# Performance work log

Measured on AMD Instinct MI355X. Metric: run time of the kernel, lower is better.

## Reference

```python
import jax, jax.numpy as jnp
import numpy as np

B, HW, E = 64, 14, 512   # batch, feature-map side, encoder_dim
A = D = M = 512          # attention_dim, decoder_dim, embed_dim
V = 1000                 # vocab_size
L = 257                  # max caption length -> T = 256 decode steps


def setup_inputs() -> dict:
    key = jax.random.key(0)
    ks = jax.random.split(key, 16)
    def w(k, shape, s=0.05):
        return jax.random.normal(k, shape, dtype=jnp.float32) * s
    encoder_out = jax.random.normal(ks[0], (B, HW, HW, E), dtype=jnp.float32)
    encoded_captions = jax.random.randint(ks[1], (B, L), 0, V)
    caption_lengths = jax.random.randint(ks[2], (B, 1), 2, L + 1)
    caption_lengths = caption_lengths.at[0, 0].set(L)  # ensure max(decode_lengths) == L-1
    return dict(
        encoder_out=encoder_out,
        encoded_captions=encoded_captions,
        caption_lengths=caption_lengths,
        emb=w(ks[3], (V, M), 0.1),
        enc_att_w=w(ks[4], (A, E)), enc_att_b=jnp.zeros((A,), jnp.float32),
        dec_att_w=w(ks[5], (A, D)), dec_att_b=jnp.zeros((A,), jnp.float32),
        full_att_w=w(ks[6], (1, A)), full_att_b=jnp.zeros((1,), jnp.float32),
        W_ih=w(ks[7], (4 * D, M + E)), b_ih=jnp.zeros((4 * D,), jnp.float32),
        W_hh=w(ks[8], (4 * D, D)), b_hh=jnp.zeros((4 * D,), jnp.float32),
        init_h_w=w(ks[9], (D, E)), init_h_b=jnp.zeros((D,), jnp.float32),
        init_c_w=w(ks[10], (D, E)), init_c_b=jnp.zeros((D,), jnp.float32),
        f_beta_w=w(ks[11], (E, D)), f_beta_b=jnp.zeros((E,), jnp.float32),
        fc_w=w(ks[12], (V, D), 0.1), fc_b=jnp.zeros((V,), jnp.float32),
    )


def _forward(encoder_out, emb, enc_att_w, enc_att_b, dec_att_w, dec_att_b,
             full_att_w, full_att_b, W_ih, b_ih, W_hh, b_hh,
             init_h_w, init_h_b, init_c_w, init_c_b,
             f_beta_w, f_beta_b, fc_w, fc_b,
             encoded_captions, caption_lengths):
    Bn = encoder_out.shape[0]
    En = encoder_out.shape[-1]
    enc = encoder_out.reshape(Bn, -1, En)            # [B, P, E]
    lens = caption_lengths[:, 0]
    sort_ind = jnp.argsort(-lens)                    # descending caption length
    lens = lens[sort_ind]
    enc = enc[sort_ind]
    caps = encoded_captions[sort_ind]
    embs = emb[caps]                                 # [B, L, M]
    mean_enc = enc.mean(axis=1)
    h0 = mean_enc @ init_h_w.T + init_h_b            # [B, D]
    c0 = mean_enc @ init_c_w.T + init_c_b
    att1 = enc @ enc_att_w.T + enc_att_b             # [B, P, A] (loop-invariant)
    dec_len = lens - 1
    T = caps.shape[1] - 1
    embs_seq = jnp.transpose(embs[:, :T, :], (1, 0, 2))  # [T, B, M]

    def step(carry, xs):
        h, c = carry
        t, emb_t = xs
        # soft attention (full batch; torch slices to active rows, masked below)
        att2 = h @ dec_att_w.T + dec_att_b                                   # [B, A]
        e = jnp.einsum('bpa,a->bp', jax.nn.relu(att1 + att2[:, None, :]),
                       full_att_w[0]) + full_att_b[0]                        # [B, P]
        alpha = jax.nn.softmax(e, axis=1)
        awe = jnp.einsum('bpe,bp->be', enc, alpha)                           # [B, E]
        gate = jax.nn.sigmoid(h @ f_beta_w.T + f_beta_b)
        x = jnp.concatenate([emb_t, gate * awe], axis=1)                     # [B, M+E]
        # LSTMCell
        gates = x @ W_ih.T + b_ih + h @ W_hh.T + b_hh
        i, f, g, o = jnp.split(gates, 4, axis=1)
        c_new = jax.nn.sigmoid(f) * c + jax.nn.sigmoid(i) * jnp.tanh(g)
        h_new = jax.nn.sigmoid(o) * jnp.tanh(c_new)
        m = (t < dec_len).astype(h.dtype)[:, None]                           # active mask
        h2 = m * h_new + (1 - m) * h
        c2 = m * c_new + (1 - m) * c
        preds = (h_new @ fc_w.T + fc_b) * m   # dropout is identity in eval
        return (h2, c2), (preds, alpha * m)

    (_, _), (preds, alphas) = jax.lax.scan(step, (h0, c0), (jnp.arange(T), embs_seq))
    predictions = jnp.transpose(preds, (1, 0, 2))   # [B, T, V]
    alphas = jnp.transpose(alphas, (1, 0, 2))       # [B, T, P]
    return predictions, caps, alphas, sort_ind


def reference(encoder_out, encoded_captions, caption_lengths, emb,
              enc_att_w, enc_att_b, dec_att_w, dec_att_b, full_att_w, full_att_b,
              W_ih, b_ih, W_hh, b_hh, init_h_w, init_h_b, init_c_w, init_c_b,
              f_beta_w, f_beta_b, fc_w, fc_b):
    return _forward(encoder_out, emb, enc_att_w, enc_att_b, dec_att_w, dec_att_b,
                    full_att_w, full_att_b, W_ih, b_ih, W_hh, b_hh,
                    init_h_w, init_h_b, init_c_w, init_c_b,
                    f_beta_w, f_beta_b, fc_w, fc_b,
                    encoded_captions, caption_lengths)
```

## Files before the change

### kernel.cpp

```cpp
#include <hip/hip_runtime.h>
#include <cstdint>
#include <cstddef>

#define NBLK 256
#define NTHR 512
#define B_ 64
#define P_ 196
#define E_ 512
#define A_ 512
#define D_ 512
#define M_ 512
#define V_ 1000
#define L_ 257
#define T_ 256

#define OUT_PRED  0
#define OUT_CAPS  (B_*T_*V_)
#define OUT_ALPHA (OUT_CAPS + B_*L_)
#define OUT_SORT  (OUT_ALPHA + B_*T_*P_)

typedef _Float16 h2 __attribute__((ext_vector_type(2)));
typedef _Float16 f16x8 __attribute__((ext_vector_type(8)));
typedef float f32x4 __attribute__((ext_vector_type(4)));

struct KP {
  const float* enc; const int* caps; const int* clen;
  const float* emb;
  const float* eaw; const float* eab;
  const float* daw; const float* dab;
  const float* faw; const float* fab;
  const float* wih; const float* bih;
  const float* whh; const float* bhh;
  const float* ihw; const float* ihb;
  const float* icw; const float* icb;
  const float* fbw; const float* fbb;
  const float* fcw; const float* fcb;
  float* out;
  int* bar; int* flb; int* gf;
  int* sort_ind; int* dec_len;
  float* mnT; float* hA; float* hB; float* hnG;
  float* a2G; float* gateG; float* aweQ; float* eG; float* att1;
  unsigned* wA2; unsigned* wG2;
};

__device__ __forceinline__ float sigf(float x){ return 1.f/(1.f+__expf(-x)); }
__device__ __forceinline__ float tanhf_(float x){
  float ax = fabsf(x);
  float e = __expf(-2.f*ax);
  float r = (1.f-e)/(1.f+e);
  return x < 0.f ? -r : r;
}
__device__ __forceinline__ unsigned short f2bf(float x){
  unsigned u = __float_as_uint(x);
  unsigned r = (u + 0x7fffu + ((u >> 16) & 1u)) >> 16;
  return (unsigned short)r;
}
__device__ __forceinline__ float fdot2f(h2 a, h2 b, float c){
#if __has_builtin(__builtin_amdgcn_fdot2)
  return __builtin_amdgcn_fdot2(a, b, c, false);
#else
  return c + (float)a.x*(float)b.x + (float)a.y*(float)b.y;
#endif
}
__device__ __forceinline__ unsigned packh2(float a, float b){
  h2 v; v.x = (_Float16)a; v.y = (_Float16)b;
  return __builtin_bit_cast(unsigned, v);
}
__device__ __forceinline__ h2 ash2(unsigned u){ return __builtin_bit_cast(h2, u); }
__device__ __forceinline__ f16x8 asf8(uint4 u){ return __builtin_bit_cast(f16x8, u); }

#define LD_A(p)     __hip_atomic_load((p), __ATOMIC_RELAXED, __HIP_MEMORY_SCOPE_AGENT)
#define ST_A(p,v)   __hip_atomic_store((p),(v), __ATOMIC_RELAXED, __HIP_MEMORY_SCOPE_AGENT)
#define ST_REL(p,v) __hip_atomic_store((p),(v), __ATOMIC_RELEASE, __HIP_MEMORY_SCOPE_AGENT)
#define FAA(p)      __hip_atomic_fetch_add((p),1, __ATOMIC_RELAXED, __HIP_MEMORY_SCOPE_AGENT)
__device__ __forceinline__ float ldg_c(const float* p){
  return __hip_atomic_load(p, __ATOMIC_RELAXED, __HIP_MEMORY_SCOPE_AGENT);
}
__device__ __forceinline__ float2 ldg2_c(const float* p){
  unsigned long long u = __hip_atomic_load((const unsigned long long*)p,
                       __ATOMIC_RELAXED, __HIP_MEMORY_SCOPE_AGENT);
  return __builtin_bit_cast(float2, u);
}
__device__ __forceinline__ void stg_c(float* p, float v){
  __hip_atomic_store(p, v, __ATOMIC_RELAXED, __HIP_MEMORY_SCOPE_AGENT);
}

__device__ __forceinline__ void gridbar(int* bar, int blk){
  __syncthreads();
  if (threadIdx.x == 0){
    __builtin_amdgcn_fence(__ATOMIC_RELEASE, "agent");
    int s = LD_A(&bar[144]);
    int* leaf = &bar[(blk & 7)*16];
    if (FAA(leaf) == 31){
      ST_A(leaf, 0);
      if (FAA(&bar[128]) == 7){
        ST_A(&bar[128], 0);
        ST_REL(&bar[144], s+1);
      }
    }
    while (LD_A(&bar[144]) == s) __builtin_amdgcn_s_sleep(2);
    __builtin_amdgcn_fence(__ATOMIC_ACQUIRE, "agent");
  }
  __syncthreads();
}

__device__ __forceinline__ void octbar(int* fl, int O, int r, int ep){
  __syncthreads();
  if (threadIdx.x == 0) ST_A(&fl[O*64 + r], ep);
  if (threadIdx.x < 32){
    while (LD_A(&fl[O*64 + (int)threadIdx.x]) < ep) __builtin_amdgcn_s_sleep(2);
  }
  asm volatile("" ::: "memory");
  __syncthreads();
}

template<int KSW>
__device__ __forceinline__ void gemv_mfma(const uint4* __restrict__ wct,
                                          const uint4* __restrict__ x4,
                                          float* redW, int lane, int wave){
  constexpr int KST = KSW*8;
  f32x4 d0 = {0.f,0.f,0.f,0.f}, d1 = d0, d2 = d0, d3 = d0;
  const int rowc = lane & 7;
  const int lg = lane >> 4;
  #pragma unroll 2
  for (int ks = 0; ks < KSW; ks++){
    const int ksg = wave*KSW + ks;
    uint4 braw = x4[(ksg*4 + lg)*8 + rowc];
    f16x8 bf = asf8(braw);
    uint4 a0 = wct[(0*KST + ksg)*64 + lane];
    uint4 a1 = wct[(1*KST + ksg)*64 + lane];
    uint4 a2 = wct[(2*KST + ksg)*64 + lane];
    uint4 a3 = wct[(3*KST + ksg)*64 + lane];
    d0 = __builtin_amdgcn_mfma_f32_16x16x32_f16(asf8(a0), bf, d0, 0, 0, 0);
    d1 = __builtin_amdgcn_mfma_f32_16x16x32_f16(asf8(a1), bf, d1, 0, 0, 0);
    d2 = __builtin_amdgcn_mfma_f32_16x16x32_f16(asf8(a2), bf, d2, 0, 0, 0);
    d3 = __builtin_amdgcn_mfma_f32_16x16x32_f16(asf8(a3), bf, d3, 0, 0, 0);
  }
  const int j = lane & 15;
  if (j < 8){
    const int ib = (lane >> 4) * 4;
    #pragma unroll
    for (int r = 0; r < 4; r++){
      redW[wave*512 + (( 0 + ib + r)*8) + j] = d0[r];
      redW[wave*512 + ((16 + ib + r)*8) + j] = d1[r];
      redW[wave*512 + ((32 + ib + r)*8) + j] = d2[r];
      redW[wave*512 + ((48 + ib + r)*8) + j] = d3[r];
    }
  }
}

__global__ __launch_bounds__(NTHR, 2) void dec_kernel(KP p){
  __shared__ __align__(16) char smem_raw[151104];
  unsigned short* att1L = (unsigned short*)smem_raw;
  unsigned* encT2  = (unsigned*)(smem_raw + 50176);
  float* fwL       = (float*)(smem_raw + 105472);
  float* cL        = (float*)(smem_raw + 107520);
  int*   sbL       = (int*)(smem_raw + 108032);
  char* SCR        = smem_raw + 108096;
  uint4* xH8_4     = (uint4*)SCR;
  float* redW      = (float*)(SCR + 24576);
  float* gLs       = (float*)(SCR + 40960);
  float* a2L       = (float*)SCR;
  float* gateL     = (float*)(SCR + 2048);
  float* eL        = (float*)(SCR + 4096);
  float* alphaL    = (float*)(SCR + 5120);
  unsigned* alpha2L= (unsigned*)(SCR + 6144);

  const int blk  = blockIdx.x;
  const int tid  = threadIdx.x;
  const int lane = tid & 63;
  const int wave = tid >> 6;
  const int b    = blk >> 2;
  const int q    = blk & 3;
  const int ct   = blk & 31;
  const int bt   = blk >> 5;

  if (blk == 0){
    if (tid < B_){
      int lb = p.clen[tid];
      int rank = 0;
      for (int j = 0; j < B_; j++){
        int lj = p.clen[j];
        rank += (lj > lb) || (lj == lb && j < tid);
      }
      p.sort_ind[rank] = tid;
      p.dec_len[rank]  = lb - 1;
      p.out[OUT_SORT + rank] = (float)tid;
    }
    __syncthreads();
    for (int idx = tid; idx < B_*L_; idx += NTHR){
      int bb = idx / L_;
      int l = idx - bb*L_;
      int sbv = p.sort_ind[bb];
      p.out[OUT_CAPS + idx] = (float)p.caps[sbv*L_ + l];
    }
  }
  gridbar(p.bar, blk);

  const int sb  = p.sort_ind[b];
  const int dlb = p.dec_len[b];

  for (int task = blk; task < 260; task += NBLK){
    if (task < 196){
      const int r0 = task*64;
      float* wL = (float*)smem_raw;
      float* eLt = (float*)smem_raw + 512*33;
      const int tx = tid & 31, ty = tid >> 5;
      float acc[4][16];
      #pragma unroll
      for (int i=0;i<4;i++)
        #pragma unroll
        for (int j=0;j<16;j++) acc[i][j] = 0.f;
      for (int k0 = 0; k0 < 512; k0 += 32){
        __syncthreads();
        for (int i = tid; i < 512*32; i += NTHR){
          int a = i >> 5, kk = i & 31;
          wL[a*33 + kk] = p.eaw[a*512 + k0 + kk];
        }
        for (int i = tid; i < 64*32; i += NTHR){
          int rl = i >> 5, kk = i & 31;
          int r = r0 + rl;
          int bb = r / 196;
          int pp = r - bb*196;
          int sbv = p.sort_ind[bb];
          eLt[rl*33 + kk] = p.enc[((size_t)sbv*196 + pp)*512 + k0 + kk];
        }
        __syncthreads();
        for (int kk = 0; kk < 32; kk++){
          float ev[4];
          #pragma unroll
          for (int ii=0;ii<4;ii++) ev[ii] = eLt[(ty*4+ii)*33 + kk];
          #pragma unroll
          for (int jj=0;jj<16;jj++){
            float wv = wL[(tx + 32*jj)*33 + kk];
            #pragma unroll
            for (int ii=0;ii<4;ii++) acc[ii][jj] = fmaf(ev[ii], wv, acc[ii][jj]);
          }
        }
      }
      #pragma unroll
      for (int jj=0;jj<16;jj++){
        int a = tx + 32*jj;
        float bbv = p.eab[a];
        #pragma unroll
        for (int ii=0;ii<4;ii++){
          int r = r0 + ty*4 + ii;
          p.att1[(size_t)r*512 + a] = acc[ii][jj] + bbv;
        }
      }
      __syncthreads();
    } else {
      int bb = task - 196;
      int sbv = p.sort_ind[bb];
      const float* eb = p.enc + (size_t)sbv*P_*E_;
      for (int e = tid; e < E_; e += NTHR){
        float s = 0.f;
        for (int pp = 0; pp < P_; pp++) s += eb[pp*E_ + e];
        p.mnT[bb*512 + e] = s * (1.f/196.f);
      }
    }
  }
  gridbar(p.bar, blk);

  for (int idx = tid; idx < 49*512; idx += NTHR){
    int pp = idx >> 9, a = idx & 511;
    att1L[idx] = f2bf(p.att1[((size_t)(b*196 + q*49 + pp))*512 + a]);
  }
  for (int i = tid; i < 512*25; i += NTHR){
    int p2 = i >> 9, e = i & 511;
    int pr0 = q*49 + 2*p2;
    float e0 = p.enc[((size_t)sb*196 + pr0)*512 + e];
    float e1 = (2*p2+1 < 49) ? p.enc[((size_t)sb*196 + pr0 + 1)*512 + e] : 0.f;
    encT2[e*27 + p2] = packh2(e0, e1);
  }
  fwL[tid] = p.faw[tid];
  if (tid < 8)       sbL[tid]     = p.sort_ind[bt*8 + tid];
  else if (tid < 16) sbL[tid]     = p.dec_len[bt*8 + (tid-8)];
  {
    int gidx = blk*512 + tid;
    int l = gidx & 63, ks = (gidx >> 6) & 15, ctmt = gidx >> 10;
    int cg = (ctmt >> 2)*64 + (ctmt & 3)*16 + (l & 15);
    int k  = ks*32 + ((l >> 4) << 3);
    uint4 o = {0u,0u,0u,0u};
    const float* src = nullptr;
    if (cg < 512)        src = p.daw + (size_t)cg*512 + k;
    else if (cg < 1024)  src = p.fbw + (size_t)(cg-512)*512 + k;
    else if (cg < 2024)  src = p.fcw + (size_t)(cg-1024)*512 + k;
    if (src){
      const float4* s4 = (const float4*)src;
      float4 f0 = s4[0], f1 = s4[1];
      o.x = packh2(f0.x,f0.y); o.y = packh2(f0.z,f0.w);
      o.z = packh2(f1.x,f1.y); o.w = packh2(f1.z,f1.w);
    }
    ((uint4*)p.wA2)[gidx] = o;
  }
  for (int s = 0; s < 3; s++){
    int gidx = blk*1536 + s*512 + tid;
    int l = gidx & 63, ks = (gidx >> 6) % 48, ctmt = gidx / 3072;
    int cg = (ctmt >> 2)*64 + (ctmt & 3)*16 + (l & 15);
    int jj = cg >> 2, g = cg & 3;
    int k  = ks*32 + ((l >> 4) << 3);
    const float* src = (k < 1024) ? p.wih + (size_t)(g*512+jj)*1024 + k
                                  : p.whh + (size_t)(g*512+jj)*512 + (k-1024);
    const float4* s4 = (const float4*)src;
    float4 f0 = s4[0], f1 = s4[1];
    uint4 o;
    o.x = packh2(f0.x,f0.y); o.y = packh2(f0.z,f0.w);
    o.z = packh2(f1.x,f1.y); o.w = packh2(f1.z,f1.w);
    ((uint4*)p.wG2)[gidx] = o;
  }
  if (tid < 128){
    int jj = tid >> 3, bb2 = tid & 7;
    int b8 = bt*8 + bb2, jg = ct*16 + jj;
    const float* mrow = p.mnT + b8*512;
    const float* hw = p.ihw + (size_t)jg*512;
    const float* cw = p.icw + (size_t)jg*512;
    float ah = 0.f, ac = 0.f;
    for (int k = 0; k < 512; k++){ ah = fmaf(hw[k], mrow[k], ah); ac = fmaf(cw[k], mrow[k], ac); }
    stg_c(&p.hA[b8*512 + jg], ah + p.ihb[jg]);
    cL[jj*8 + bb2] = ac + p.icb[jg];
  }
  gridbar(p.bar, blk);

  const float fab0 = p.fab[0];
  int ep = 0;

  for (int t = 0; t < T_; t++){
    const float* hR = (t & 1) ? p.hB : p.hA;
    float*       hW = (t & 1) ? p.hA : p.hB;

    if (ct < 16 || t > 0){
      {
        const float* xsrc = (ct < 16) ? hR : p.hnG;
        int cc = tid >> 3, r = tid & 7;
        const float* src = xsrc + (size_t)(bt*8 + r)*512 + cc*8;
        float2 v0 = ldg2_c(src), v1 = ldg2_c(src+2), v2 = ldg2_c(src+4), v3 = ldg2_c(src+6);
        uint4 o;
        o.x = packh2(v0.x,v0.y); o.y = packh2(v1.x,v1.y);
        o.z = packh2(v2.x,v2.y); o.w = packh2(v3.x,v3.y);
        xH8_4[tid] = o;
      }
      __syncthreads();
      gemv_mfma<2>((const uint4*)p.wA2 + (size_t)ct*4096, xH8_4, redW, lane, wave);
      __syncthreads();
      {
        float s = 0.f;
        #pragma unroll
        for (int w8 = 0; w8 < 8; w8++) s += redW[w8*512 + tid];
        int c_local = tid >> 3, j = tid & 7, b8 = bt*8 + j;
        if (ct < 16){
          int vcl = ct*64 + c_local;
          if (vcl < 512) stg_c(&p.a2G[b8*512 + vcl], s + p.dab[vcl]);
          else           stg_c(&p.gateG[b8*512 + (vcl-512)], sigf(s + p.fbb[vcl-512]));
        } else {
          int v2i = (ct-16)*64 + c_local;
          if (v2i < 1000){
            bool mm = (t-1) < sbL[8 + j];
            p.out[OUT_PRED + ((size_t)b8*T_ + (t-1))*V_ + v2i] = mm ? (s + p.fcb[v2i]) : 0.f;
          }
        }
      }
    }
    octbar(p.flb, bt, ct, ++ep);

    {
      a2L[tid]   = ldg_c(&p.a2G[b*512 + tid]);
      gateL[tid] = ldg_c(&p.gateG[b*512 + tid]);
      __syncthreads();
      {
        float4 aA = ((float4*)a2L)[lane*2], aB = ((float4*)a2L)[lane*2+1];
        float4 fA = ((float4*)fwL)[lane*2], fB = ((float4*)fwL)[lane*2+1];
        for (int pp = wave; pp < 49; pp += 8){
          uint4 raw = ((const uint4*)att1L)[pp*64 + lane];
          float s =
            fmaxf(__uint_as_float(raw.x << 16)        + aA.x, 0.f)*fA.x +
            fmaxf(__uint_as_float(raw.x & 0xffff0000u)+ aA.y, 0.f)*fA.y +
            fmaxf(__uint_as_float(raw.y << 16)        + aA.z, 0.f)*fA.z +
            fmaxf(__uint_as_float(raw.y & 0xffff0000u)+ aA.w, 0.f)*fA.w +
            fmaxf(__uint_as_float(raw.z << 16)        + aB.x, 0.f)*fB.x +
            fmaxf(__uint_as_float(raw.z & 0xffff0000u)+ aB.y, 0.f)*fB.y +
            fmaxf(__uint_as_float(raw.w << 16)        + aB.z, 0.f)*fB.z +
            fmaxf(__uint_as_float(raw.w & 0xffff0000u)+ aB.w, 0.f)*fB.w;
          #pragma unroll
          for (int o = 32; o > 0; o >>= 1) s += __shfl_down(s, o);
          if (lane == 0) stg_c(&p.eG[b*256 + q*49 + pp], s + fab0);
        }
      }
      __syncthreads();
      if (tid == 0) ST_A(&p.gf[b*16 + q], t+1);
      if (tid < 4){
        while (LD_A(&p.gf[b*16 + tid]) < t+1) __builtin_amdgcn_s_sleep(1);
      }
      asm volatile("" ::: "memory");
      __syncthreads();
      if (tid < 196) eL[tid] = ldg_c(&p.eG[b*256 + tid]);
      __syncthreads();
      if (wave == 0){
        float mx = -1e30f;
        for (int i = lane; i < P_; i += 64) mx = fmaxf(mx, eL[i]);
        #pragma unroll
        for (int o = 32; o > 0; o >>= 1) mx = fmaxf(mx, __shfl_xor(mx, o));
        float sum = 0.f;
        for (int i = lane; i < P_; i += 64){
          float ex = __expf(eL[i] - mx);
          alphaL[i] = ex;
          sum += ex;
        }
        #pragma unroll
        for (int o = 32; o > 0; o >>= 1) sum += __shfl_xor(sum, o);
        float inv = 1.f / sum;
        for (int i = lane; i < P_; i += 64) alphaL[i] *= inv;
      }
      __syncthreads();
      {
        bool mb = t < dlb;
        if (tid < 49)
          p.out[OUT_ALPHA + ((size_t)b*T_ + t)*P_ + q*49 + tid] = mb ? alphaL[q*49 + tid] : 0.f;
        if (tid < 25){
          float a0 = alphaL[q*49 + 2*tid];
          float a1 = (2*tid+1 < 49) ? alphaL[q*49 + 2*tid + 1] : 0.f;
          alpha2L[tid] = packh2(a0, a1);
        }
      }
      __syncthreads();
      {
        const unsigned* ec = encT2 + tid*27;
        float s = 0.f;
        #pragma unroll 5
        for (int p2 = 0; p2 < 25; p2++)
          s = fdot2f(ash2(ec[p2]), ash2(alpha2L[p2]), s);
        stg_c(&p.aweQ[((size_t)b*4 + q)*512 + tid], gateL[tid]*s);
      }
    }
    octbar(p.flb, bt, ct, ++ep);

    {
      {
        int cc = tid >> 3, r = tid & 7;
        int b8 = bt*8 + r;
        {
          int cap = p.caps[sbL[r]*L_ + t];
          const float4* er = (const float4*)(p.emb + (size_t)cap*M_ + cc*8);
          float4 f0 = er[0], f1 = er[1];
          uint4 o;
          o.x = packh2(f0.x,f0.y); o.y = packh2(f0.z,f0.w);
          o.z = packh2(f1.x,f1.y); o.w = packh2(f1.z,f1.w);
          xH8_4[tid] = o;
        }
        {
          const float* aw = p.aweQ + (size_t)b8*4*512 + cc*8;
          float a8[8];
          #pragma unroll
          for (int e = 0; e < 8; e += 2){
            float2 q0 = ldg2_c(aw + 0*512 + e);
            float2 q1 = ldg2_c(aw + 1*512 + e);
            float2 q2 = ldg2_c(aw + 2*512 + e);
            float2 q3 = ldg2_c(aw + 3*512 + e);
            a8[e]   = (q0.x + q1.x) + (q2.x + q3.x);
            a8[e+1] = (q0.y + q1.y) + (q2.y + q3.y);
          }
          uint4 o;
          o.x = packh2(a8[0],a8[1]); o.y = packh2(a8[2],a8[3]);
          o.z = packh2(a8[4],a8[5]); o.w = packh2(a8[6],a8[7]);
          xH8_4[512 + tid] = o;
        }
        {
          const float* hs = hR + (size_t)b8*512 + cc*8;
          float2 v0 = ldg2_c(hs), v1 = ldg2_c(hs+2), v2 = ldg2_c(hs+4), v3 = ldg2_c(hs+6);
          uint4 o;
          o.x = packh2(v0.x,v0.y); o.y = packh2(v1.x,v1.y);
          o.z = packh2(v2.x,v2.y); o.w = packh2(v3.x,v3.y);
          xH8_4[1024 + tid] = o;
        }
      }
      __syncthreads();
      gemv_mfma<6>((const uint4*)p.wG2 + (size_t)ct*12288, xH8_4, redW, lane, wave);
      __syncthreads();
      {
        float s = 0.f;
        #pragma unroll
        for (int w8 = 0; w8 < 8; w8++) s += redW[w8*512 + tid];
        gLs[(tid & 7)*64 + (tid >> 3)] = s;
      }
      __syncthreads();
      if (tid < 128){
        int jj = tid >> 3, bb2 = tid & 7;
        int b8 = bt*8 + bb2, jg = ct*16 + jj;
        float g0 = gLs[bb2*64 + jj*4+0] + p.bih[jg]        + p.bhh[jg];
        float g1 = gLs[bb2*64 + jj*4+1] + p.bih[512 + jg]  + p.bhh[512 + jg];
        float g2 = gLs[bb2*64 + jj*4+2] + p.bih[1024 + jg] + p.bhh[1024 + jg];
        float g3 = gLs[bb2*64 + jj*4+3] + p.bih[1536 + jg] + p.bhh[1536 + jg];
        float i_s = sigf(g0), f_s = sigf(g1), g_t = tanhf_(g2), o_s = sigf(g3);
        float c_old = cL[jj*8 + bb2];
        float c_new = f_s*c_old + i_s*g_t;
        float h_new = o_s*tanhf_(c_new);
        bool m = t < sbL[8 + bb2];
        float h_old = ldg_c(&hR[b8*512 + jg]);
        cL[jj*8 + bb2] = m ? c_new : c_old;
        stg_c(&p.hnG[b8*512 + jg], h_new);
        stg_c(&hW[b8*512 + jg], m ? h_new : h_old);
      }
    }
    octbar(p.flb, bt, ct, ++ep);
  }

  if (ct >= 16){
    {
      int cc = tid >> 3, r = tid & 7;
      const float* src = p.hnG + (size_t)(bt*8 + r)*512 + cc*8;
      float2 v0 = ldg2_c(src), v1 = ldg2_c(src+2), v2 = ldg2_c(src+4), v3 = ldg2_c(src+6);
      uint4 o;
      o.x = packh2(v0.x,v0.y); o.y = packh2(v1.x,v1.y);
      o.z = packh2(v2.x,v2.y); o.w = packh2(v3.x,v3.y);
      xH8_4[tid] = o;
    }
    __syncthreads();
    gemv_mfma<2>((const uint4*)p.wA2 + (size_t)ct*4096, xH8_4, redW, lane, wave);
    __syncthreads();
    {
      float s = 0.f;
      #pragma unroll
      for (int w8 = 0; w8 < 8; w8++) s += redW[w8*512 + tid];
      int c_local = tid >> 3, j = tid & 7, b8 = bt*8 + j;
      int v2i = (ct-16)*64 + c_local;
      if (v2i < 1000){
        bool mm = (T_-1) < sbL[8 + j];
        p.out[OUT_PRED + ((size_t)b8*T_ + (T_-1))*V_ + v2i] = mm ? (s + p.fcb[v2i]) : 0.f;
      }
    }
  }
}

extern "C" void kernel_launch(void* const* d_in, const int* in_sizes, int n_in,
                              void* d_out, int out_size, void* d_ws, size_t ws_size,
                              hipStream_t stream){
  (void)in_sizes; (void)n_in; (void)out_size; (void)ws_size;
  KP p;
  p.enc  = (const float*)d_in[0];
  p.caps = (const int*)  d_in[1];
  p.clen = (const int*)  d_in[2];
  p.emb  = (const float*)d_in[3];
  p.eaw  = (const float*)d_in[4];  p.eab = (const float*)d_in[5];
  p.daw  = (const float*)d_in[6];  p.dab = (const float*)d_in[7];
  p.faw  = (const float*)d_in[8];  p.fab = (const float*)d_in[9];
  p.wih  = (const float*)d_in[10]; p.bih = (const float*)d_in[11];
  p.whh  = (const float*)d_in[12]; p.bhh = (const float*)d_in[13];
  p.ihw  = (const float*)d_in[14]; p.ihb = (const float*)d_in[15];
  p.icw  = (const float*)d_in[16]; p.icb = (const float*)d_in[17];
  p.fbw  = (const float*)d_in[18]; p.fbb = (const float*)d_in[19];
  p.fcw  = (const float*)d_in[20]; p.fcb = (const float*)d_in[21];
  p.out  = (float*)d_out;

  char* ws = (char*)d_ws;
  size_t off = 0;
  p.bar = (int*)(ws + off); off += 1024;
  p.flb = (int*)(ws + off); off += 8*64*4;
  p.gf  = (int*)(ws + off); off += 64*16*4;
  size_t zero_bytes = off;
  p.sort_ind = (int*)(ws + off); off += 64*4;
  p.dec_len  = (int*)(ws + off); off += 64*4;
  off = (off + 255) & ~(size_t)255;
  p.mnT   = (float*)(ws + off); off += (size_t)B_*512*4;
  p.hA    = (float*)(ws + off); off += (size_t)B_*512*4;
  p.hB    = (float*)(ws + off); off += (size_t)B_*512*4;
  p.hnG   = (float*)(ws + off); off += (size_t)B_*512*4;
  p.a2G   = (float*)(ws + off); off += (size_t)B_*512*4;
  p.gateG = (float*)(ws + off); off += (size_t)B_*512*4;
  p.aweQ  = (float*)(ws + off); off += (size_t)B_*4*512*4;
  p.eG    = (float*)(ws + off); off += (size_t)B_*256*4;
  p.att1  = (float*)(ws + off); off += (size_t)B_*P_*A_*4;
  p.wA2   = (unsigned*)(ws + off); off += (size_t)256*2048*4;
  p.wG2   = (unsigned*)(ws + off); off += (size_t)768*2048*4;

  hipMemsetAsync(ws, 0, zero_bytes, stream);

  void* args[] = { (void*)&p };
  hipLaunchCooperativeKernel((const void*)dec_kernel,
                             dim3(NBLK), dim3(NTHR), args, 0, stream);
}
```

Measured before the change: 5.634 ms.

## Keep per-block GEMV weight fragments resident in registers across all decode steps

```diff
diff --git a/kernel.cpp b/kernel.cpp
--- a/kernel.cpp
+++ b/kernel.cpp
@@ -40,7 +40,6 @@
   int* sort_ind; int* dec_len;
   float* mnT; float* hA; float* hB; float* hnG;
   float* a2G; float* gateG; float* aweQ; float* eG; float* att1;
-  unsigned* wA2; unsigned* wG2;
 };
 
 __device__ __forceinline__ float sigf(float x){ return 1.f/(1.f+__expf(-x)); }
@@ -115,26 +114,20 @@
 }
 
 template<int KSW>
-__device__ __forceinline__ void gemv_mfma(const uint4* __restrict__ wct,
+__device__ __forceinline__ void gemv_regs(const uint4 (&wfr)[4][KSW],
                                           const uint4* __restrict__ x4,
                                           float* redW, int lane, int wave){
-  constexpr int KST = KSW*8;
   f32x4 d0 = {0.f,0.f,0.f,0.f}, d1 = d0, d2 = d0, d3 = d0;
   const int rowc = lane & 7;
   const int lg = lane >> 4;
-  #pragma unroll 2
+  #pragma unroll
   for (int ks = 0; ks < KSW; ks++){
     const int ksg = wave*KSW + ks;
-    uint4 braw = x4[(ksg*4 + lg)*8 + rowc];
-    f16x8 bf = asf8(braw);
-    uint4 a0 = wct[(0*KST + ksg)*64 + lane];
-    uint4 a1 = wct[(1*KST + ksg)*64 + lane];
-    uint4 a2 = wct[(2*KST + ksg)*64 + lane];
-    uint4 a3 = wct[(3*KST + ksg)*64 + lane];
-    d0 = __builtin_amdgcn_mfma_f32_16x16x32_f16(asf8(a0), bf, d0, 0, 0, 0);
-    d1 = __builtin_amdgcn_mfma_f32_16x16x32_f16(asf8(a1), bf, d1, 0, 0, 0);
-    d2 = __builtin_amdgcn_mfma_f32_16x16x32_f16(asf8(a2), bf, d2, 0, 0, 0);
-    d3 = __builtin_amdgcn_mfma_f32_16x16x32_f16(asf8(a3), bf, d3, 0, 0, 0);
+    f16x8 bf = asf8(x4[(ksg*4 + lg)*8 + rowc]);
+    d0 = __builtin_amdgcn_mfma_f32_16x16x32_f16(asf8(wfr[0][ks]), bf, d0, 0, 0, 0);
+    d1 = __builtin_amdgcn_mfma_f32_16x16x32_f16(asf8(wfr[1][ks]), bf, d1, 0, 0, 0);
+    d2 = __builtin_amdgcn_mfma_f32_16x16x32_f16(asf8(wfr[2][ks]), bf, d2, 0, 0, 0);
+    d3 = __builtin_amdgcn_mfma_f32_16x16x32_f16(asf8(wfr[3][ks]), bf, d3, 0, 0, 0);
   }
   const int j = lane & 15;
   if (j < 8){
@@ -276,38 +269,44 @@
   fwL[tid] = p.faw[tid];
   if (tid < 8)       sbL[tid]     = p.sort_ind[bt*8 + tid];
   else if (tid < 16) sbL[tid]     = p.dec_len[bt*8 + (tid-8)];
+  uint4 wa[4][2];
+  uint4 wg[4][6];
   {
-    int gidx = blk*512 + tid;
-    int l = gidx & 63, ks = (gidx >> 6) & 15, ctmt = gidx >> 10;
-    int cg = (ctmt >> 2)*64 + (ctmt & 3)*16 + (l & 15);
-    int k  = ks*32 + ((l >> 4) << 3);
-    uint4 o = {0u,0u,0u,0u};
-    const float* src = nullptr;
-    if (cg < 512)        src = p.daw + (size_t)cg*512 + k;
-    else if (cg < 1024)  src = p.fbw + (size_t)(cg-512)*512 + k;
-    else if (cg < 2024)  src = p.fcw + (size_t)(cg-1024)*512 + k;
-    if (src){
-      const float4* s4 = (const float4*)src;
-      float4 f0 = s4[0], f1 = s4[1];
-      o.x = packh2(f0.x,f0.y); o.y = packh2(f0.z,f0.w);
-      o.z = packh2(f1.x,f1.y); o.w = packh2(f1.z,f1.w);
-    }
-    ((uint4*)p.wA2)[gidx] = o;
-  }
-  for (int s = 0; s < 3; s++){
-    int gidx = blk*1536 + s*512 + tid;
-    int l = gidx & 63, ks = (gidx >> 6) % 48, ctmt = gidx / 3072;
-    int cg = (ctmt >> 2)*64 + (ctmt & 3)*16 + (l & 15);
-    int jj = cg >> 2, g = cg & 3;
-    int k  = ks*32 + ((l >> 4) << 3);
-    const float* src = (k < 1024) ? p.wih + (size_t)(g*512+jj)*1024 + k
-                                  : p.whh + (size_t)(g*512+jj)*512 + (k-1024);
-    const float4* s4 = (const float4*)src;
-    float4 f0 = s4[0], f1 = s4[1];
-    uint4 o;
-    o.x = packh2(f0.x,f0.y); o.y = packh2(f0.z,f0.w);
-    o.z = packh2(f1.x,f1.y); o.w = packh2(f1.z,f1.w);
-    ((uint4*)p.wG2)[gidx] = o;
+    const int cgb = ct*64 + (lane & 15);
+    const int kof = (lane >> 4) << 3;
+    #pragma unroll
+    for (int mt = 0; mt < 4; mt++){
+      int cg = cgb + mt*16;
+      #pragma unroll
+      for (int ks = 0; ks < 2; ks++){
+        int k = (wave*2 + ks)*32 + kof;
+        uint4 o = {0u,0u,0u,0u};
+        const float* src = nullptr;
+        if (cg < 512)        src = p.daw + (size_t)cg*512 + k;
+        else if (cg < 1024)  src = p.fbw + (size_t)(cg-512)*512 + k;
+        else if (cg < 2024)  src = p.fcw + (size_t)(cg-1024)*512 + k;
+        if (src){
+          const float4* s4 = (const float4*)src;
+          float4 f0 = s4[0], f1 = s4[1];
+          o.x = packh2(f0.x,f0.y); o.y = packh2(f0.z,f0.w);
+          o.z = packh2(f1.x,f1.y); o.w = packh2(f1.z,f1.w);
+        }
+        wa[mt][ks] = o;
+      }
+      int jj = cg >> 2, g = cg & 3;
+      #pragma unroll
+      for (int ks = 0; ks < 6; ks++){
+        int k = (wave*6 + ks)*32 + kof;
+        const float* src = (k < 1024) ? p.wih + (size_t)(g*512+jj)*1024 + k
+                                      : p.whh + (size_t)(g*512+jj)*512 + (k-1024);
+        const float4* s4 = (const float4*)src;
+        float4 f0 = s4[0], f1 = s4[1];
+        uint4 o;
+        o.x = packh2(f0.x,f0.y); o.y = packh2(f0.z,f0.w);
+        o.z = packh2(f1.x,f1.y); o.w = packh2(f1.z,f1.w);
+        wg[mt][ks] = o;
+      }
+    }
   }
   if (tid < 128){
     int jj = tid >> 3, bb2 = tid & 7;
@@ -341,7 +340,7 @@
         xH8_4[tid] = o;
       }
       __syncthreads();
-      gemv_mfma<2>((const uint4*)p.wA2 + (size_t)ct*4096, xH8_4, redW, lane, wave);
+      gemv_regs<2>(wa, xH8_4, redW, lane, wave);
       __syncthreads();
       {
         float s = 0.f;
@@ -474,7 +473,7 @@
         }
       }
       __syncthreads();
-      gemv_mfma<6>((const uint4*)p.wG2 + (size_t)ct*12288, xH8_4, redW, lane, wave);
+      gemv_regs<6>(wg, xH8_4, redW, lane, wave);
       __syncthreads();
       {
         float s = 0.f;
@@ -515,7 +514,7 @@
       xH8_4[tid] = o;
     }
     __syncthreads();
-    gemv_mfma<2>((const uint4*)p.wA2 + (size_t)ct*4096, xH8_4, redW, lane, wave);
+    gemv_regs<2>(wa, xH8_4, redW, lane, wave);
     __syncthreads();
     {
       float s = 0.f;
@@ -569,8 +568,6 @@
   p.aweQ  = (float*)(ws + off); off += (size_t)B_*4*512*4;
   p.eG    = (float*)(ws + off); off += (size_t)B_*256*4;
   p.att1  = (float*)(ws + off); off += (size_t)B_*P_*A_*4;
-  p.wA2   = (unsigned*)(ws + off); off += (size_t)256*2048*4;
-  p.wG2   = (unsigned*)(ws + off); off += (size_t)768*2048*4;
 
   hipMemsetAsync(ws, 0, zero_bytes, stream);
 
```

Result: no change. 5.617 ms (-0.3%).
